# Optimization experiments

Hardware: AMD Instinct MI355X
Metric: run time of the kernel (lower is better)

## Reference

```python
import jax, jax.numpy as jnp
import numpy as np

TOPK = 8
EPS = 1e-12  # matches torch F.normalize default eps


def setup_inputs() -> dict:
    key = jax.random.key(0)
    x = jax.random.normal(key, (8, 2048, 128), dtype=jnp.float32)
    return {"x": x}


def reference(x) -> jnp.ndarray:
    B, N, D = x.shape
    # --- pairwise dot scores on L2-normalized features (cosine similarity) ---
    norm = jnp.sqrt(jnp.sum(x * x, axis=-1, keepdims=True))
    normed = x / jnp.maximum(norm, EPS)
    scores = jnp.einsum('bnd,bmd->bnm', normed, normed)  # [B, N, N]

    # --- top-k per row -> binary adjacency via scatter ---
    _, idx = jax.lax.top_k(scores, TOPK)  # [B, N, k]
    bi = jnp.arange(B)[:, None, None]
    ni = jnp.arange(N)[None, :, None]
    adj = jnp.zeros((B, N, N), dtype=x.dtype).at[bi, ni, idx].set(1.0)

    # --- symmetrize and add self loops ---
    adj = jnp.maximum(adj, jnp.swapaxes(adj, 1, 2))
    eye = jnp.eye(N, dtype=x.dtype)
    adj = jnp.maximum(adj, eye[None, :, :])
    return adj
```

## Files before the change

### kernel.cpp

```cpp
#include <hip/hip_runtime.h>
#include <cstdint>

#define NN 2048
#define DD 128
#define BATCH 8
#define NROWS 16384
#define MARGIN 0.02f
#define CAP 64

typedef __attribute__((ext_vector_type(8))) short bf16x8;
typedef __attribute__((ext_vector_type(4))) float f32x4;
typedef unsigned long long u64;
typedef unsigned int u32;
typedef unsigned short u16;

__device__ __forceinline__ u32 bf16rne(float f) {
  u32 u = __float_as_uint(f);
  return (u + 0x7fffu + ((u >> 16) & 1u)) >> 16;
}

__global__ __launch_bounds__(256) void k_zero(float4* __restrict__ out, int n4) {
  int i = blockIdx.x * 256 + threadIdx.x;
  const int stride = gridDim.x * 256;
  const float4 z = {0.0f, 0.0f, 0.0f, 0.0f};
  for (; i < n4; i += stride) out[i] = z;
}

__global__ __launch_bounds__(256) void k_normalize(const float* __restrict__ x,
                                                   double* __restrict__ rinv,
                                                   u32* __restrict__ nb) {
  const int wave = threadIdx.x >> 6, lane = threadIdx.x & 63;
  const long long row = (long long)blockIdx.x * 4 + wave;
  float2 v = ((const float2*)(x + row * DD))[lane];
  const double d0 = v.x, d1 = v.y;
  double s = d0 * d0 + d1 * d1;
  #pragma unroll
  for (int m = 32; m >= 1; m >>= 1) s += __shfl_xor(s, m, 64);
  double den = sqrt(s); den = den > 1e-12 ? den : 1e-12;
  if (lane == 0) rinv[row] = 1.0 / den;
  double2 o; o.x = d0 / den; o.y = d1 / den;
  nb[row * (DD / 2) + lane] = bf16rne((float)o.x) | (bf16rne((float)o.y) << 16);
}

#define CXF(i, j) { const float a_ = L[i], b_ = L[j]; L[i] = fmaxf(a_, b_); L[j] = fminf(a_, b_); }
__device__ __forceinline__ void merge8f(float (&kv)[8], const float (&ov)[8]) {
  float L[8];
  #pragma unroll
  for (int i = 0; i < 8; ++i) L[i] = fmaxf(kv[i], ov[7 - i]);
  CXF(0, 4) CXF(1, 5) CXF(2, 6) CXF(3, 7)
  CXF(0, 2) CXF(1, 3) CXF(4, 6) CXF(5, 7)
  CXF(0, 1) CXF(2, 3) CXF(4, 5) CXF(6, 7)
  #pragma unroll
  for (int i = 0; i < 8; ++i) kv[i] = L[i];
}

__device__ __forceinline__ u64 make_key(double s, int col) {
  u64 u = (u64)__double_as_longlong(s);
  const u64 m = (u64)((long long)u >> 63);
  u ^= (m | 0x8000000000000000ull);
  return (u & ~2047ull) | (u64)(2047 - col);
}
__device__ __forceinline__ u64 umax64(u64 a, u64 b) { return a > b ? a : b; }
__device__ __forceinline__ u64 umin64(u64 a, u64 b) { return a > b ? b : a; }
__device__ __forceinline__ void merge8(u64 (&kv)[8], const u64 (&ov)[8]) {
  u64 L[8];
  #pragma unroll
  for (int i = 0; i < 8; ++i) L[i] = umax64(kv[i], ov[7 - i]);
#define CX(i, j) { const u64 a_ = L[i], b_ = L[j]; L[i] = umax64(a_, b_); L[j] = umin64(a_, b_); }
  CX(0, 4) CX(1, 5) CX(2, 6) CX(3, 7)
  CX(0, 2) CX(1, 3) CX(4, 6) CX(5, 7)
  CX(0, 1) CX(2, 3) CX(4, 5) CX(6, 7)
#undef CX
  #pragma unroll
  for (int i = 0; i < 8; ++i) kv[i] = L[i];
}
__device__ __forceinline__ void insert8u(u64 (&v)[8], u64 nk) {
  if (nk > v[7]) {
    v[7] = nk;
    #pragma unroll
    for (int q = 7; q >= 1; --q) {
      const u64 a = v[q - 1], b = v[q];
      const bool sw = b > a;
      v[q - 1] = sw ? b : a; v[q] = sw ? a : b;
    }
  }
}

__global__ __launch_bounds__(256) void k_gram(const u32* __restrict__ nb,
                                              u16* __restrict__ scores,
                                              u16* __restrict__ bmaxg) {
  __shared__ u16 bml[4][16][40];
  const int tid = threadIdx.x; const int w = tid >> 6; const int l = tid & 63;
  const int q = l >> 4; const int m = l & 15;
  bf16x8 pvals = {0,0,0,0,0,0,0,0}, pones = {0,0,0,0,0,0,0,0};
  if (q == 0) {
    pvals[0] = (short)(__float_as_uint((float)(m + 1)) >> 16);
    pones[0] = (short)(__float_as_uint(1.0f) >> 16);
  }
  const f32x4 z4 = {0.0f, 0.0f, 0.0f, 0.0f};
  const f32x4 pr  = __builtin_amdgcn_mfma_f32_16x16x32_bf16(pvals, pones, z4, 0, 0, 0);
  const f32x4 pr2 = __builtin_amdgcn_mfma_f32_16x16x32_bf16(pones, pvals, z4, 0, 0, 0);
  int cof[4];
  #pragma unroll
  for (int p = 0; p < 4; ++p) cof[p] = (int)pr[p] - 1;
  const int rof = (int)pr2[0] - 1;
  const bool contig = (cof[1] == cof[0] + 1) && (cof[2] == cof[0] + 2) &&
                      (cof[3] == cof[0] + 3) && ((cof[0] & 3) == 0);
  const int rowblk = blockIdx.x >> 2; const int split = blockIdx.x & 3;
  const int row0 = rowblk * 64 + 16 * w;
  const int b = rowblk >> 5; const int c0 = split * 512;
  const u32* Bb = nb + ((long long)b * NN + c0) * (DD / 2);
  bf16x8 ar[4];
  { const u32* Ap = nb + (long long)(row0 + m) * (DD / 2) + 4 * q;
    #pragma unroll
    for (int cc = 0; cc < 4; ++cc) ar[cc] = *(const bf16x8*)(Ap + 16 * cc); }
  bf16x8 bcA[4], bcB[4];
  u16* rowbase = scores + (long long)(row0 + rof) * NN + c0;

#define LOADB(DST, T) { const u32* p_ = Bb + (long long)(16 * (T) + m) * (DD / 2) + 4 * q; \
  _Pragma("unroll") for (int cc = 0; cc < 4; ++cc) DST[cc] = *(const bf16x8*)(p_ + 16 * cc); }
#define GEMM16(ACC, BC) { ACC = z4;                                                \
  _Pragma("unroll") for (int cc = 0; cc < 4; ++cc)                                 \
    ACC = __builtin_amdgcn_mfma_f32_16x16x32_bf16(BC[cc], ar[cc], ACC, 0, 0, 0); }
#define STORE4(ACC, T) { u16* sp = rowbase + 16 * (T);                             \
    if (contig) {                                                                  \
      uint2 sv;                                                                    \
      sv.x = bf16rne(ACC[0]) | (bf16rne(ACC[1]) << 16);                            \
      sv.y = bf16rne(ACC[2]) | (bf16rne(ACC[3]) << 16);                            \
      *(uint2*)(sp + cof[0]) = sv;                                                 \
    } else {                                                                       \
      sp[cof[0]] = (u16)bf16rne(ACC[0]); sp[cof[1]] = (u16)bf16rne(ACC[1]);        \
      sp[cof[2]] = (u16)bf16rne(ACC[2]); sp[cof[3]] = (u16)bf16rne(ACC[3]);        \
    }                                                                              \
    float bm_ = fmaxf(fmaxf(ACC[0], ACC[1]), fmaxf(ACC[2], ACC[3]));               \
    bm_ = fmaxf(bm_, __shfl_xor(bm_, 16, 64));                                     \
    bm_ = fmaxf(bm_, __shfl_xor(bm_, 32, 64));                                     \
    if (q == 0) bml[w][m][T] = (u16)bf16rne(bm_); }

  LOADB(bcA, 0)
  for (int t = 0; t < 32; t += 2) {
    LOADB(bcB, t + 1)
    { f32x4 acc; GEMM16(acc, bcA) STORE4(acc, t) }
    if (t + 2 < 32) LOADB(bcA, t + 2)
    { f32x4 acc; GEMM16(acc, bcB) STORE4(acc, t + 1) }
  }
#undef LOADB
#undef GEMM16
#undef STORE4

  __syncthreads();
  {
    const int row2 = tid >> 2;
    const int seg  = tid & 3;
    const int wsrc = row2 >> 4, msrc = row2 & 15;
    uint4 v = *(const uint4*)&bml[wsrc][msrc][seg * 8];
    *(uint4*)(bmaxg + ((long long)split * 16384 + rowblk * 64 + row2) * 32 + seg * 8) = v;
  }
}

__global__ __launch_bounds__(256) void k_topk_exact(const u16* __restrict__ scores,
                                                    const u16* __restrict__ bmaxg,
                                                    const float* __restrict__ x,
                                                    const double* __restrict__ rinv,
                                                    float* __restrict__ out) {
  __shared__ u32 scnt[4];
  __shared__ u32 sblkn[4];
  __shared__ u32 sblk[4][CAP];
  __shared__ u32 scand[4][CAP];

  const int w = threadIdx.x >> 6, l = threadIdx.x & 63;
  const int r = blockIdx.x * 4 + w;
  const int n = r & (NN - 1);
  const long long brow = r - n;

  if (l == 0) { scnt[w] = 0u; sblkn[w] = 0u; }

  const int s_ = l >> 4, idx_ = l & 15;
  const u32 bm2 = *(const u32*)(bmaxg + ((long long)s_ * 16384 + r) * 32 + 2 * idx_);
  const float b0 = __uint_as_float(bm2 << 16);
  const float b1 = __uint_as_float(bm2 & 0xFFFF0000u);
  const int blk0 = s_ * 32 + 2 * idx_;
  float mx = fmaxf(b0, b1);

  float kv8[8];
  {
    const float o  = __shfl_xor(mx, 1, 64);
    const float h2 = fmaxf(mx, o), l2 = fminf(mx, o);
    const float p0 = __shfl_xor(h2, 2, 64), p1 = __shfl_xor(l2, 2, 64);
    const float m0 = fmaxf(h2, p0);
    const float xx = fminf(h2, p0);
    const float yy = fmaxf(l2, p1);
    const float m3 = fminf(l2, p1);
    const float m1 = fmaxf(xx, yy);
    const float m2 = fminf(xx, yy);
    const float q0 = __shfl_xor(m0, 4, 64), q1 = __shfl_xor(m1, 4, 64);
    const float q2 = __shfl_xor(m2, 4, 64), q3 = __shfl_xor(m3, 4, 64);
    float L[8] = {m0, m1, m2, m3, q3, q2, q1, q0};
    CXF(0, 4) CXF(1, 5) CXF(2, 6) CXF(3, 7)
    CXF(0, 2) CXF(1, 3) CXF(4, 6) CXF(5, 7)
    CXF(0, 1) CXF(2, 3) CXF(4, 5) CXF(6, 7)
    #pragma unroll
    for (int s = 0; s < 8; ++s) kv8[s] = L[s];
    #pragma unroll
    for (int mk = 8; mk <= 32; mk <<= 1) {
      float ov[8];
      #pragma unroll
      for (int s = 0; s < 8; ++s) ov[s] = __shfl_xor(kv8[s], mk, 64);
      merge8f(kv8, ov);
    }
  }
  const float th = kv8[7] - MARGIN;

  if (b0 >= th) { const u32 id = atomicAdd(&sblkn[w], 1u); if (id < CAP) sblk[w][id] = (u32)blk0; }
  if (b1 >= th) { const u32 id = atomicAdd(&sblkn[w], 1u); if (id < CAP) sblk[w][id] = (u32)(blk0 + 1); }

  int c;
  const int nbq = (int)sblkn[w];
  const u16* rowp = scores + (long long)r * NN;
  if (nbq <= CAP) {
    for (int i = 0; i < nbq; i += 4) {
      const int bi = i + s_;
      const u32 blk = (bi < nbq) ? sblk[w][bi] : sblk[w][0];
      const int col = (int)blk * 16 + idx_;
      const float v = __uint_as_float((u32)rowp[col] << 16);
      if (bi < nbq && v >= th) {
        const u32 id = atomicAdd(&scnt[w], 1u);
        if (id < CAP) scand[w][id] = (u32)col;
      }
    }
    c = (int)scnt[w];
  } else {
    c = CAP + 1;
  }

  const float2 a2 = ((const float2*)(x + (long long)r * DD))[l];
  const double ri = rinv[r];
  u64 kv[8];
  #pragma unroll
  for (int s = 0; s < 8; ++s) kv[s] = 0ull;

  if (c <= CAP) {
    for (int i = 0; i < c; i += 4) {
      float2 vv[4]; int col[4];
      #pragma unroll
      for (int g = 0; g < 4; ++g) {
        const int idx = i + g;
        col[g] = (idx < c) ? ((int)scand[w][idx] & (NN - 1)) : 0;
        vv[g] = ((const float2*)(x + (brow + col[g]) * DD))[l];
      }
      #pragma unroll
      for (int g = 0; g < 4; ++g) {
        double d = fma((double)a2.x, (double)vv[g].x, (double)a2.y * (double)vv[g].y);
        #pragma unroll
        for (int mk = 1; mk <= 32; mk <<= 1) d += __shfl_xor(d, mk, 64);
        if (i + g < c) insert8u(kv, make_key(d * ri * rinv[brow + col[g]], col[g]));
      }
    }
  } else {
    for (int base = 0; base < NN; base += 64) {
      const int col = base + l;
      const float* ap = x + (long long)r * DD;
      const float* cp = x + (brow + col) * DD;
      double d = 0.0;
      for (int kk = 0; kk < 64; ++kk) {
        const float2 av = ((const float2*)ap)[kk];
        const float2 bv = ((const float2*)cp)[kk];
        d = fma((double)av.x, (double)bv.x, fma((double)av.y, (double)bv.y, d));
      }
      d = d * ri * rinv[brow + col];
      u64 one[8];
      one[0] = make_key(d, col);
      #pragma unroll
      for (int s = 1; s < 8; ++s) one[s] = 0ull;
      #pragma unroll
      for (int mk = 1; mk <= 32; mk <<= 1) {
        u64 ov[8];
        #pragma unroll
        for (int s = 0; s < 8; ++s) ov[s] = __shfl_xor(one[s], mk, 64);
        merge8(one, ov);
      }
      merge8(kv, one);
    }
  }

  const long long orow = (long long)r * NN;
  const long long obase = brow * NN;
  if (l == 8) out[orow + n] = 1.0f;
  #pragma unroll
  for (int s = 0; s < 8; ++s) {
    const int mcol = 2047 - (int)(kv[s] & 2047ull);
    if (l == s) {
      out[orow + mcol] = 1.0f;
      out[obase + (long long)mcol * NN + n] = 1.0f;
    }
  }
}

extern "C" void kernel_launch(void* const* d_in, const int* in_sizes, int n_in,
                              void* d_out, int out_size, void* d_ws, size_t ws_size,
                              hipStream_t stream) {
  const float* x = (const float*)d_in[0];
  float* out = (float*)d_out;
  char* ws = (char*)d_ws;
  u32* nb = (u32*)ws;
  double* rinv = (double*)(ws + 4194304);
  u16* scores = (u16*)(ws + 4325376);
  u16* bmaxg = (u16*)(ws + 71434240);

  hipLaunchKernelGGL(k_zero, dim3(4096), dim3(256), 0, stream,
                     (float4*)out, out_size / 4);
  hipLaunchKernelGGL(k_normalize, dim3(NROWS / 4), dim3(256), 0, stream, x, rinv, nb);
  hipLaunchKernelGGL(k_gram, dim3(1024), dim3(256), 0, stream, nb, scores, bmaxg);
  hipLaunchKernelGGL(k_topk_exact, dim3(NROWS / 4), dim3(256), 0, stream, scores, bmaxg, x, rinv, out);
}
```

Before: 270.7 us.

## Retile k_gram so each wave computes 64 rows by 128 columns

Each wave in the Gram kernel now keeps A fragments for all 64 block rows in registers and sweeps a 128-column slice of its own. Before, it held 16 rows and swept 512 columns. Each B tile load now feeds four MFMA row groups instead of one, which cuts global/L2 traffic for B by about four times per block. Block-max staging is now per-wave, so the __syncthreads is gone. In exchange, the wave holds four times as many A registers, which may raise VGPR pressure and reduce occupancy.

```diff
diff --git a/kernel.cpp b/kernel.cpp
--- a/kernel.cpp
+++ b/kernel.cpp
@@ -89,7 +89,7 @@
 __global__ __launch_bounds__(256) void k_gram(const u32* __restrict__ nb,
                                               u16* __restrict__ scores,
                                               u16* __restrict__ bmaxg) {
-  __shared__ u16 bml[4][16][40];
+  __shared__ u16 bml[4][64][16];
   const int tid = threadIdx.x; const int w = tid >> 6; const int l = tid & 63;
   const int q = l >> 4; const int m = l & 15;
   bf16x8 pvals = {0,0,0,0,0,0,0,0}, pones = {0,0,0,0,0,0,0,0};
@@ -107,22 +107,28 @@
   const bool contig = (cof[1] == cof[0] + 1) && (cof[2] == cof[0] + 2) &&
                       (cof[3] == cof[0] + 3) && ((cof[0] & 3) == 0);
   const int rowblk = blockIdx.x >> 2; const int split = blockIdx.x & 3;
-  const int row0 = rowblk * 64 + 16 * w;
-  const int b = rowblk >> 5; const int c0 = split * 512;
-  const u32* Bb = nb + ((long long)b * NN + c0) * (DD / 2);
-  bf16x8 ar[4];
-  { const u32* Ap = nb + (long long)(row0 + m) * (DD / 2) + 4 * q;
+  const int row0 = rowblk * 64;
+  const int b = rowblk >> 5;
+  const int c0w = split * 512 + w * 128;
+  const u32* Bb = nb + ((long long)b * NN + c0w) * (DD / 2);
+
+  bf16x8 ar4[4][4];
+  #pragma unroll
+  for (int rf = 0; rf < 4; ++rf) {
+    const u32* Ap = nb + (long long)(row0 + 16 * rf + m) * (DD / 2) + 4 * q;
     #pragma unroll
-    for (int cc = 0; cc < 4; ++cc) ar[cc] = *(const bf16x8*)(Ap + 16 * cc); }
+    for (int cc = 0; cc < 4; ++cc) ar4[rf][cc] = *(const bf16x8*)(Ap + 16 * cc);
+  }
+  u16* rowb[4];
+  #pragma unroll
+  for (int rf = 0; rf < 4; ++rf)
+    rowb[rf] = scores + (long long)(row0 + 16 * rf + rof) * NN + c0w;
+
   bf16x8 bcA[4], bcB[4];
-  u16* rowbase = scores + (long long)(row0 + rof) * NN + c0;
 
 #define LOADB(DST, T) { const u32* p_ = Bb + (long long)(16 * (T) + m) * (DD / 2) + 4 * q; \
   _Pragma("unroll") for (int cc = 0; cc < 4; ++cc) DST[cc] = *(const bf16x8*)(p_ + 16 * cc); }
-#define GEMM16(ACC, BC) { ACC = z4;                                                \
-  _Pragma("unroll") for (int cc = 0; cc < 4; ++cc)                                 \
-    ACC = __builtin_amdgcn_mfma_f32_16x16x32_bf16(BC[cc], ar[cc], ACC, 0, 0, 0); }
-#define STORE4(ACC, T) { u16* sp = rowbase + 16 * (T);                             \
+#define STOREB(ACC, T, RF) { u16* sp = rowb[RF] + 16 * (T);                        \
     if (contig) {                                                                  \
       uint2 sv;                                                                    \
       sv.x = bf16rne(ACC[0]) | (bf16rne(ACC[1]) << 16);                            \
@@ -135,26 +141,30 @@
     float bm_ = fmaxf(fmaxf(ACC[0], ACC[1]), fmaxf(ACC[2], ACC[3]));               \
     bm_ = fmaxf(bm_, __shfl_xor(bm_, 16, 64));                                     \
     bm_ = fmaxf(bm_, __shfl_xor(bm_, 32, 64));                                     \
-    if (q == 0) bml[w][m][T] = (u16)bf16rne(bm_); }
+    if (q == 0) bml[w][16 * (RF) + m][T] = (u16)bf16rne(bm_); }
+#define TILE(BC, T) {                                                              \
+    _Pragma("unroll") for (int rf = 0; rf < 4; ++rf) {                             \
+      f32x4 acc = z4;                                                              \
+      _Pragma("unroll") for (int cc = 0; cc < 4; ++cc)                             \
+        acc = __builtin_amdgcn_mfma_f32_16x16x32_bf16(BC[cc], ar4[rf][cc], acc, 0, 0, 0); \
+      STOREB(acc, T, rf)                                                           \
+    } }
 
   LOADB(bcA, 0)
-  for (int t = 0; t < 32; t += 2) {
+  #pragma unroll
+  for (int t = 0; t < 8; t += 2) {
     LOADB(bcB, t + 1)
-    { f32x4 acc; GEMM16(acc, bcA) STORE4(acc, t) }
-    if (t + 2 < 32) LOADB(bcA, t + 2)
-    { f32x4 acc; GEMM16(acc, bcB) STORE4(acc, t + 1) }
+    TILE(bcA, t)
+    if (t + 2 < 8) LOADB(bcA, t + 2)
+    TILE(bcB, t + 1)
   }
 #undef LOADB
-#undef GEMM16
-#undef STORE4
-
-  __syncthreads();
+#undef STOREB
+#undef TILE
+
   {
-    const int row2 = tid >> 2;
-    const int seg  = tid & 3;
-    const int wsrc = row2 >> 4, msrc = row2 & 15;
-    uint4 v = *(const uint4*)&bml[wsrc][msrc][seg * 8];
-    *(uint4*)(bmaxg + ((long long)split * 16384 + rowblk * 64 + row2) * 32 + seg * 8) = v;
+    const uint4 v = *(const uint4*)&bml[w][l][0];
+    *(uint4*)(bmaxg + ((long long)split * 16384 + row0 + l) * 32 + w * 8) = v;
   }
 }
 
```

New measurement: 254.3 us. 1.06x faster.
